# Optimization experiments

Hardware: AMD Instinct MI355X
Metric: run time of the kernel (lower is better)

The kernel has to match this reference:

```python
import jax, jax.numpy as jnp
import numpy as np
import math

S, B, H, NH, I, L, V, BK, MP = 512, 8, 768, 12, 2304, 4, 16384, 32, 512
DH = H // NH   # 64
DV = I // NH   # 192
EPS = 1e-7
SCALE = 1.0 / math.sqrt(3 * DH)


def make_log_bucket_position(relative_pos, bucket_size, max_position):
    sign = np.sign(relative_pos)
    mid = bucket_size // 2
    abs_pos = np.where((relative_pos < mid) & (relative_pos > -mid),
                       mid - 1,
                       np.clip(np.abs(relative_pos), None, max_position - 1))
    log_pos = np.ceil(np.log(abs_pos / mid) / math.log((max_position - 1) / mid) * (mid - 1)).astype(np.int64) + mid
    bucket_pos = np.where(abs_pos <= mid, relative_pos, log_pos * sign).astype(np.int64)
    return bucket_pos


def layer_norm(x, eps=EPS):
    m = jnp.mean(x, axis=-1, keepdims=True)
    v = jnp.var(x, axis=-1, keepdims=True)
    return (x - m) / jnp.sqrt(v + eps)


def setup_inputs() -> dict:
    key = jax.random.key(0)
    ks = jax.random.split(key, 10)
    std = math.sqrt(2.0 / (5.0 * H))
    inp = {}
    inp['input_ids'] = jax.random.randint(ks[0], (S, B), 0, V, dtype=jnp.int32)
    inp['attention_mask'] = jnp.zeros((B, 1, 1, S), dtype=bool)
    rel = np.arange(S)[:, None] - np.arange(S)[None, :]
    rel = make_log_bucket_position(rel, BK, MP)
    inp['position_indices'] = jnp.asarray(BK - 1 + rel, dtype=jnp.int32)  # [S,S] in [0, 2*BK-2]
    inp['word_emb'] = jax.random.normal(ks[1], (V, H), jnp.float32) * std
    inp['rel_emb'] = jax.random.normal(ks[2], (2 * BK - 1, H), jnp.float32) * std
    inp['rel_ln_w'] = jnp.ones((H,), jnp.float32)
    inp['rel_ln_b'] = jnp.zeros((H,), jnp.float32)
    inp['Wv'] = jax.random.normal(ks[3], (L, 2 * I, H), jnp.float32) * std
    inp['Wqk'] = jax.random.normal(ks[4], (L, 2 * H, H), jnp.float32) * std
    inp['bqk'] = jnp.zeros((L, 2 * H), jnp.float32)
    inp['Wo'] = jax.random.normal(ks[5], (L, H, I), jnp.float32) * std
    inp['l_skip'] = jnp.zeros((L, I), jnp.float32)
    return inp


def attention_glu_layer(x, mask, rel, pos_idx, Wv, Wqk, bqk, Wo, l_skip):
    # x: [S,B,H]; rel: [2*BK-1, H]; mask: [B,1,1,S] bool (True = masked)
    h = layer_norm(x)
    vg = jnp.einsum('sbh,ih->sbi', h, Wv)                  # [S,B,2I]
    value, gate = jnp.split(vg, 2, axis=-1)
    gate = jax.nn.gelu(gate, approximate=False)
    value_skip = jax.nn.gelu(value, approximate=False)
    qk = jnp.einsum('sbh,ih->sbi', h, Wqk) + bqk            # [S,B,2H]
    q, k = jnp.split(qk, 2, axis=-1)
    # relative position projections
    pos = rel @ Wqk.T + bqk                                 # [2*BK-1, 2H]
    pos = pos[pos_idx]                                      # [S,S,2H]
    q_pos, k_pos = jnp.split(pos, 2, axis=-1)
    q_pos = q_pos.reshape(S, S, NH, DH)
    k_pos = k_pos.reshape(S, S, NH, DH)
    q4 = q.reshape(S, B, NH, DH)
    k4 = k.reshape(S, B, NH, DH)
    v4 = value.reshape(S, B, NH, DV)
    scores = jnp.einsum('qbhd,kbhd->bhqk', q4, k4) * SCALE
    scores = scores + jnp.einsum('qbhd,qkhd->bhqk', q4, k_pos) * SCALE
    scores = scores + jnp.einsum('kbhd,qkhd->bhqk', k4, q_pos) * SCALE
    scores = jnp.where(mask, -jnp.inf, scores)
    probs = jax.nn.softmax(scores, axis=-1)
    probs = jnp.where(mask, 0.0, probs)
    ctx = jnp.einsum('bhqk,kbhv->qbhv', probs, v4).reshape(S, B, I)
    ctx = ctx + jax.nn.sigmoid(l_skip) * value_skip
    ctx = ctx * gate
    ctx = layer_norm(ctx)
    out = jnp.einsum('sbi,hi->sbh', ctx, Wo)
    return x + out


def reference(input_ids, attention_mask, position_indices, word_emb, rel_emb,
              rel_ln_w, rel_ln_b, Wv, Wqk, bqk, Wo, l_skip):
    x = layer_norm(word_emb[input_ids])                      # [S,B,H]
    rel = layer_norm(rel_emb) * rel_ln_w + rel_ln_b          # [2*BK-1, H]
    for l in range(L):
        x = attention_glu_layer(x, attention_mask, rel, position_indices,
                                Wv[l], Wqk[l], bqk[l], Wo[l], l_skip[l])
    return x
```

## Files before the change

kernel.cpp:

```cpp
#include <hip/hip_runtime.h>
#include <hip/hip_bf16.h>
#include <math.h>

#define S 512
#define B 8
#define H 768
#define NH 12
#define DH 64
#define DV 192
#define II 2304
#define NL 4
#define SCALE 0.07216878364870322f
#define EPS 1e-7f

#define NW0 (2*II*H)
#define NW1 (2*H*H)
#define NW2 (H*II)

typedef __attribute__((ext_vector_type(8))) short short8;
typedef __attribute__((ext_vector_type(4))) float f32x4;

__device__ __forceinline__ float b2f(ushort u){
  union { float f; unsigned int u; } v; v.u = ((unsigned int)u) << 16; return v.f;
}
__device__ __forceinline__ ushort f2b(float f){
  union { float f; unsigned int u; } v; v.f = f;
  unsigned int u = v.u;
  return (ushort)((u + 0x7fffu + ((u >> 16) & 1u)) >> 16);
}
__device__ __forceinline__ float gelu_f(float x){
  return 0.5f * x * (1.0f + erff(x * 0.70710678118654752f));
}
__device__ __forceinline__ void async_copy16(const ushort* g, ushort* l){
  __builtin_amdgcn_global_load_lds(
      (const __attribute__((address_space(1))) void*)g,
      (__attribute__((address_space(3))) void*)l, 16, 0, 0);
}

__device__ __forceinline__ void block_sum2(float& s, float& s2, float* red, int t){
  #pragma unroll
  for(int off=32; off>=1; off>>=1){ s += __shfl_xor(s, off); s2 += __shfl_xor(s2, off); }
  int w = t >> 6;
  if((t & 63) == 0){ red[w] = s; red[4 + w] = s2; }
  __syncthreads();
  s  = red[0] + red[1] + red[2] + red[3];
  s2 = red[4] + red[5] + red[6] + red[7];
}

__global__ __launch_bounds__(256)
void f2b3_kernel(const float* __restrict__ in0, const float* __restrict__ in1,
                 const float* __restrict__ in2, ushort* __restrict__ out){
  int i = (blockIdx.x * 256 + threadIdx.x) * 4;
  const float* src; int off;
  if(i < NW0){ src = in0; off = i; }
  else if(i < NW0+NW1){ src = in1; off = i - NW0; }
  else { src = in2; off = i - NW0 - NW1; }
  float4 v = *(const float4*)(src + off);
  __attribute__((aligned(8))) ushort tmp[4] = { f2b(v.x), f2b(v.y), f2b(v.z), f2b(v.w) };
  *(uint2*)(out + i) = *(const uint2*)tmp;
}

__global__ __launch_bounds__(256)
void embed_ln_kernel(const int* __restrict__ ids, const float* __restrict__ wemb,
                     float* __restrict__ x)
{
  __shared__ float red[8];
  const int sb = blockIdx.x, t = threadIdx.x;
  const float* row = wemb + (size_t)ids[sb] * H;
  float v0 = row[t], v1 = row[t+256], v2 = row[t+512];
  float s = v0+v1+v2, s2 = v0*v0+v1*v1+v2*v2;
  block_sum2(s, s2, red, t);
  float mean = s * (1.0f/H);
  float rstd = rsqrtf(s2*(1.0f/H) - mean*mean + EPS);
  float* xo = x + (size_t)sb * H;
  xo[t]     = (v0-mean)*rstd;
  xo[t+256] = (v1-mean)*rstd;
  xo[t+512] = (v2-mean)*rstd;
}

__global__ __launch_bounds__(256)
void rel_ln_kernel(const float* __restrict__ rel_emb, const float* __restrict__ w,
                   const float* __restrict__ bia, ushort* __restrict__ outb)
{
  __shared__ float red[8];
  const int j = blockIdx.x, t = threadIdx.x;
  const float* row = rel_emb + (size_t)j * H;
  float v0=row[t], v1=row[t+256], v2=row[t+512];
  float s=v0+v1+v2, s2=v0*v0+v1*v1+v2*v2;
  block_sum2(s,s2,red,t);
  float mean = s*(1.0f/H);
  float rstd = rsqrtf(s2*(1.0f/H)-mean*mean+EPS);
  ushort* o = outb + (size_t)j*H;
  o[t]     = f2b((v0-mean)*rstd * w[t]     + bia[t]);
  o[t+256] = f2b((v1-mean)*rstd * w[t+256] + bia[t+256]);
  o[t+512] = f2b((v2-mean)*rstd * w[t+512] + bia[t+512]);
}

__global__ __launch_bounds__(256)
void ln_x_kernel(const float* __restrict__ x, ushort* __restrict__ h)
{
  __shared__ float red[8];
  const int sb = blockIdx.x, t = threadIdx.x;
  const float* row = x + (size_t)sb * H;
  float v0 = row[t], v1 = row[t+256], v2 = row[t+512];
  float s = v0+v1+v2, s2 = v0*v0+v1*v1+v2*v2;
  block_sum2(s, s2, red, t);
  float mean = s * (1.0f/H);
  float rstd = rsqrtf(s2*(1.0f/H) - mean*mean + EPS);
  ushort* o = h + (size_t)sb * H;
  o[t]     = f2b((v0-mean)*rstd);
  o[t+256] = f2b((v1-mean)*rstd);
  o[t+512] = f2b((v2-mean)*rstd);
}

__global__ __launch_bounds__(256)
void bucket_kernel(const int* __restrict__ pidx, unsigned char* __restrict__ buk){
  int r = blockIdx.x*256 + threadIdx.x;
  int rel = r - 511;
  int v = 0;
  if(rel <= 0)          v = pidx[-rel];
  else if(rel <= 511)   v = pidx[511*S + (511-rel)];
  buk[r] = (unsigned char)v;
}

__global__ __launch_bounds__(256)
void gemm_nt64(const ushort* __restrict__ A, const ushort* __restrict__ Bw,
               const float* __restrict__ bias, ushort* __restrict__ Cout,
               int M, int N, int K)
{
  __shared__ ushort As[64][40];
  __shared__ ushort Bs[64][40];
  const int n0 = blockIdx.x * 64, m0 = blockIdx.y * 64;
  const int t = threadIdx.x;
  const int lrow = t >> 2, lk = (t & 3) * 8;
  const int lane = t & 63, w = t >> 6, lr = lane & 15, lq = lane >> 4;
  const int wr = (w >> 1) * 32, wc = (w & 1) * 32;
  f32x4 z = {0.f,0.f,0.f,0.f};
  f32x4 acc[2][2] = {{z,z},{z,z}};
  const int arow = m0 + lrow;
  const ushort* aptr = A  + (size_t)arow * K + lk;
  const ushort* bptr = Bw + (size_t)(n0 + lrow) * K + lk;
  for(int k0 = 0; k0 < K; k0 += 32){
    short8 av = {0,0,0,0,0,0,0,0};
    if(arow < M) av = *(const short8*)(aptr + k0);
    short8 bv = *(const short8*)(bptr + k0);
    __syncthreads();
    *(short8*)&As[lrow][lk] = av;
    *(short8*)&Bs[lrow][lk] = bv;
    __syncthreads();
    short8 a0 = *(const short8*)&As[wr + lr][lq * 8];
    short8 a1 = *(const short8*)&As[wr + 16 + lr][lq * 8];
    short8 b0 = *(const short8*)&Bs[wc + lr][lq * 8];
    short8 b1 = *(const short8*)&Bs[wc + 16 + lr][lq * 8];
    acc[0][0] = __builtin_amdgcn_mfma_f32_16x16x32_bf16(a0, b0, acc[0][0], 0,0,0);
    acc[0][1] = __builtin_amdgcn_mfma_f32_16x16x32_bf16(a0, b1, acc[0][1], 0,0,0);
    acc[1][0] = __builtin_amdgcn_mfma_f32_16x16x32_bf16(a1, b0, acc[1][0], 0,0,0);
    acc[1][1] = __builtin_amdgcn_mfma_f32_16x16x32_bf16(a1, b1, acc[1][1], 0,0,0);
  }
  #pragma unroll
  for(int i=0;i<2;i++){
    #pragma unroll
    for(int j=0;j<2;j++){
      #pragma unroll
      for(int r=0;r<4;r++){
        int m = m0 + wr + i*16 + lq*4 + r;
        int n = n0 + wc + j*16 + lr;
        if(m >= M) continue;
        float v = acc[i][j][r];
        if(bias) v += bias[n];
        Cout[(size_t)m*N + n] = f2b(v);
      }
    }
  }
}

template<int OUT_MODE>
__global__ __launch_bounds__(256)
void gemm128(const ushort* __restrict__ A, const ushort* __restrict__ Bw,
             const float* __restrict__ bias, void* __restrict__ Cout,
             int M, int N, int K)
{
  __shared__ ushort As[2][128*32];
  __shared__ ushort Bs[2][128*32];
  const int t = threadIdx.x, w = t>>6, lane = t&63, lr = lane&15, lq = lane>>4;
  const int m0 = blockIdx.y*128, n0 = blockIdx.x*128;
  const int wr = (w>>1)*64, wc = (w&1)*64;
  const int srow = (w*2)*16 + (lane>>2);
  const int sk = (lane&3)*8;
  const ushort* aG = A  + (size_t)(m0+srow)*K + sk;
  const ushort* bG = Bw + (size_t)(n0+srow)*K + sk;
  f32x4 z = {0.f,0.f,0.f,0.f};
  f32x4 acc[4][4] = {{z,z,z,z},{z,z,z,z},{z,z,z,z},{z,z,z,z}};
  for(int k0 = 0; k0 < K; k0 += 64){
    __syncthreads();
    #pragma unroll
    for(int s=0;s<2;s++){
      async_copy16(aG + k0 + s*32,                 As[s] + (w*2)*512);
      async_copy16(aG + k0 + s*32 + (size_t)16*K,  As[s] + (w*2+1)*512);
      async_copy16(bG + k0 + s*32,                 Bs[s] + (w*2)*512);
      async_copy16(bG + k0 + s*32 + (size_t)16*K,  Bs[s] + (w*2+1)*512);
    }
    __syncthreads();
    #pragma unroll
    for(int s=0;s<2;s++){
      short8 af[4], bf[4];
      #pragma unroll
      for(int i=0;i<4;i++) af[i] = *(const short8*)&As[s][(wr + i*16 + lr)*32 + lq*8];
      #pragma unroll
      for(int j=0;j<4;j++) bf[j] = *(const short8*)&Bs[s][(wc + j*16 + lr)*32 + lq*8];
      #pragma unroll
      for(int i=0;i<4;i++)
        #pragma unroll
        for(int j=0;j<4;j++)
          acc[i][j] = __builtin_amdgcn_mfma_f32_16x16x32_bf16(af[i], bf[j], acc[i][j], 0,0,0);
    }
  }
  #pragma unroll
  for(int i=0;i<4;i++){
    #pragma unroll
    for(int j=0;j<4;j++){
      #pragma unroll
      for(int r=0;r<4;r++){
        int m = m0 + wr + i*16 + lq*4 + r;
        int n = n0 + wc + j*16 + lr;
        float v = acc[i][j][r];
        if(bias) v += bias[n];
        if(OUT_MODE == 0)      ((float*) Cout)[(size_t)m*N + n] = v;
        else if(OUT_MODE == 1) ((ushort*)Cout)[(size_t)m*N + n] = f2b(v);
        else                   ((float*) Cout)[(size_t)m*N + n] += v;
      }
    }
  }
}

#define VGQK_TILE(KT, CUR, SB) do {                                            \
    const int ks0_ = ((KT)+2)*64;                                              \
    const bool do_stage_ = ((KT)+2) < NT;                                      \
    if((KT) < NT-1) asm volatile("s_waitcnt vmcnt(6)" ::: "memory");           \
    else            asm volatile("s_waitcnt vmcnt(0)" ::: "memory");           \
    __builtin_amdgcn_s_barrier();                                              \
    __builtin_amdgcn_sched_barrier(0);                                         \
    short8 bfr_[4][2], afr_[2][2];                                             \
    _Pragma("unroll")                                                          \
    for(int j=0;j<4;j++)                                                       \
      _Pragma("unroll")                                                        \
      for(int ks=0;ks<2;ks++)                                                  \
        bfr_[j][ks] = *(const short8*)&(CUR)[8192 + (wn*64 + j*16 + lr)*64 + ((ks*32 + lq*8) ^ rxor)]; \
    _Pragma("unroll")                                                          \
    for(int i=0;i<2;i++)                                                       \
      _Pragma("unroll")                                                        \
      for(int ks=0;ks<2;ks++)                                                  \
        afr_[i][ks] = *(const short8*)&(CUR)[(wm*64 + i*16 + lr)*64 + ((ks*32 + lq*8) ^ rxor)]; \
    if(do_stage_){                                                             \
      async_copy16(aSrc + ks0_,                (SB) + dA);                     \
      async_copy16(aSrc + (size_t)64*K + ks0_, (SB) + 4096 + dA);              \
      async_copy16(bSrc + ks0_,                (SB) + 8192 + dA);              \
    }                                                                          \
    __builtin_amdgcn_s_barrier();                                              \
    asm volatile("s_waitcnt lgkmcnt(0)" ::: "memory");                         \
    __builtin_amdgcn_sched_barrier(0);                                         \
    __builtin_amdgcn_s_setprio(1);                                             \
    _Pragma("unroll")                                                          \
    for(int i=0;i<2;i++)                                                       \
      _Pragma("unroll")                                                        \
      for(int j=0;j<4;j++)                                                     \
        _Pragma("unroll")                                                      \
        for(int ks=0;ks<2;ks++)                                                \
          acc[i][j] = __builtin_amdgcn_mfma_f32_16x16x32_bf16(afr_[i][ks], bfr_[j][ks], acc[i][j], 0,0,0); \
    __builtin_amdgcn_s_setprio(0);                                             \
    __builtin_amdgcn_s_barrier();                                              \
    __builtin_amdgcn_sched_barrier(0);                                         \
    short8 afr2_[2][2];                                                        \
    _Pragma("unroll")                                                          \
    for(int i=0;i<2;i++)                                                       \
      _Pragma("unroll")                                                        \
      for(int ks=0;ks<2;ks++)                                                  \
        afr2_[i][ks] = *(const short8*)&(CUR)[(wm*64 + (2+i)*16 + lr)*64 + ((ks*32 + lq*8) ^ rxor)]; \
    if(do_stage_){                                                             \
      async_copy16(bSrc + (size_t)64*K + ks0_,  (SB) + 12288 + dA);            \
      async_copy16(bSrc + (size_t)128*K + ks0_, (SB) + 16384 + dA);            \
      async_copy16(bSrc + (size_t)192*K + ks0_, (SB) + 20480 + dA);            \
    }                                                                          \
    __builtin_amdgcn_s_barrier();                                              \
    asm volatile("s_waitcnt lgkmcnt(0)" ::: "memory");                         \
    __builtin_amdgcn_sched_barrier(0);                                         \
    __builtin_amdgcn_s_setprio(1);                                             \
    _Pragma("unroll")                                                          \
    for(int i=0;i<2;i++)                                                       \
      _Pragma("unroll")                                                        \
      for(int j=0;j<4;j++)                                                     \
        _Pragma("unroll")                                                      \
        for(int ks=0;ks<2;ks++)                                                \
          acc[2+i][j] = __builtin_amdgcn_mfma_f32_16x16x32_bf16(afr2_[i][ks], bfr_[j][ks], acc[2+i][j], 0,0,0); \
    __builtin_amdgcn_s_setprio(0);                                             \
  } while(0)

__global__ __launch_bounds__(512)
void gemm_vgqk8(const ushort* __restrict__ A, const ushort* __restrict__ Ww,
                const float* __restrict__ bqk, ushort* __restrict__ vg,
                ushort* __restrict__ qk)
{
  constexpr int K  = H;
  constexpr int NT = K / 64;
  __shared__ ushort buf0[24576];
  __shared__ ushort buf1[24576];
  __shared__ ushort buf2[24576];
  const int t = threadIdx.x;
  const int w = t >> 6, l = t & 63, lr = l & 15, lq = l >> 4;
  const int wm = w >> 2, wn = w & 3;
  int id = blockIdx.x;
  int swz = (id & 7) * 96 + (id >> 3);
  const int bm = swz & 31, bn = swz >> 5;
  const int m0 = bm * 128, n0 = bn * 256;

  const int srow = l >> 3;
  const int scol = ((l & 7) ^ srow) << 3;
  const ushort* aSrc = A  + (size_t)(m0 + w*8 + srow) * K + scol;
  const ushort* bSrc = Ww + (size_t)(n0 + w*8 + srow) * K + scol;
  const int dA = w * 512;
  const int rxor = (lr & 7) << 3;

  f32x4 z = {0.f,0.f,0.f,0.f};
  f32x4 acc[4][4] = {{z,z,z,z},{z,z,z,z},{z,z,z,z},{z,z,z,z}};

  async_copy16(aSrc + 0,                  buf0 + dA);
  async_copy16(aSrc + (size_t)64*K + 0,   buf0 + 4096  + dA);
  async_copy16(bSrc + 0,                  buf0 + 8192  + dA);
  async_copy16(bSrc + (size_t)64*K + 0,   buf0 + 12288 + dA);
  async_copy16(bSrc + (size_t)128*K + 0,  buf0 + 16384 + dA);
  async_copy16(bSrc + (size_t)192*K + 0,  buf0 + 20480 + dA);
  async_copy16(aSrc + 64,                 buf1 + dA);
  async_copy16(aSrc + (size_t)64*K + 64,  buf1 + 4096  + dA);
  async_copy16(bSrc + 64,                 buf1 + 8192  + dA);
  async_copy16(bSrc + (size_t)64*K + 64,  buf1 + 12288 + dA);
  async_copy16(bSrc + (size_t)128*K + 64, buf1 + 16384 + dA);
  async_copy16(bSrc + (size_t)192*K + 64, buf1 + 20480 + dA);

  for(int m3=0; m3<NT/3; m3++){
    const int kt = m3*3;
    VGQK_TILE(kt,   buf0, buf2);
    VGQK_TILE(kt+1, buf1, buf0);
    VGQK_TILE(kt+2, buf2, buf1);
  }

  const bool is_qk = (n0 >= 2*II);
  #pragma unroll
  for(int i=0;i<4;i++){
    #pragma unroll
    for(int j=0;j<4;j++){
      #pragma unroll
      for(int r=0;r<4;r++){
        int m = m0 + wm*64 + i*16 + lq*4 + r;
        int n = n0 + wn*64 + j*16 + lr;
        float v = acc[i][j][r];
        if(is_qk){
          int nq = n - 2*II;
          qk[(size_t)m*(2*H) + nq] = f2b(v + bqk[nq]);
        } else {
          vg[(size_t)m*(2*II) + n] = f2b(v);
        }
      }
    }
  }
}

__global__ __launch_bounds__(256)
void vtcpq_kernel(const ushort* __restrict__ vg, ushort* __restrict__ vt,
                  const ushort* __restrict__ qk, const ushort* __restrict__ posb,
                  ushort* __restrict__ cpT, ushort* __restrict__ cqT,
                  ushort* __restrict__ kT)
{
  const int id = blockIdx.x;
  const int t = threadIdx.x;
  __shared__ ushort tile[32][200];
  if(id < 1536){
    const int st = id & 15;
    const int hh = (id >> 4) % 12;
    const int b  = id / 192;
    {
      int sl = t >> 3, v0 = (t & 7) * 24;
      const ushort* src = vg + ((size_t)((st*32 + sl)*B + b))*(2*II) + hh*DV + v0;
      *(short8*)&tile[sl][v0]      = *(const short8*)(src);
      *(short8*)&tile[sl][v0 + 8]  = *(const short8*)(src + 8);
      *(short8*)&tile[sl][v0 + 16] = *(const short8*)(src + 16);
    }
    __syncthreads();
    if(t < DV){
      __attribute__((aligned(16))) ushort tmp[32];
      #pragma unroll
      for(int s2=0;s2<32;s2++) tmp[s2] = tile[s2][t];
      ushort* dst = vt + ((((size_t)(b*NH + hh))*16 + st)*DV + t)*32;
      #pragma unroll
      for(int c=0;c<32;c+=8) *(short8*)(dst + c) = *(const short8*)&tmp[c];
    }
  } else if(id < 2304){
    const int jid = id - 1536;
    const int kc = jid & 3;
    const int bh = (jid >> 2) % 96;
    const int which = jid / 384;
    const int bb = bh / NH, h = bh - bb*NH;
    const int w = t>>6, lane = t&63, lr = lane&15, lq = lane>>4;
    const ushort* ab = posb + (size_t)(w*16 + lr)*1536 + (which ? 0 : 768) + h*64;
    short8 a0 = *(const short8*)(ab + lq*8);
    short8 a1 = *(const short8*)(ab + 32 + lq*8);
    f32x4 z = {0.f,0.f,0.f,0.f};
    f32x4 acc[8] = {z,z,z,z,z,z,z,z};
    #pragma unroll
    for(int nt=0; nt<8; nt++){
      const int k = kc*128 + nt*16 + lr;
      const ushort* bp = qk + ((size_t)k*B + bb)*1536 + (which ? 768 : 0) + h*64;
      short8 b0 = *(const short8*)(bp + lq*8);
      short8 b1 = *(const short8*)(bp + 32 + lq*8);
      acc[nt] = __builtin_amdgcn_mfma_f32_16x16x32_bf16(a0, b0, acc[nt], 0,0,0);
      acc[nt] = __builtin_amdgcn_mfma_f32_16x16x32_bf16(a1, b1, acc[nt], 0,0,0);
    }
    ushort* outp = which ? cqT : cpT;
    #pragma unroll
    for(int nt=0; nt<8; nt++){
      #pragma unroll
      for(int r=0;r<4;r++){
        int j = w*16 + lq*4 + r;
        int k = kc*128 + nt*16 + lr;
        outp[((size_t)bh*64 + j)*512 + k] = f2b(acc[nt][r]);
      }
    }
  } else {
    const int id2 = id - 2304;
    const int bb = id2 / NH, hh = id2 - bb*NH;
    const int sl = t >> 3, d0 = (t & 7) * 8;
    const ushort* srcb = qk + (size_t)bb*1536 + H + hh*64 + d0;
    ushort* dstb = kT + ((size_t)id2*512 + sl)*64 + d0;
    #pragma unroll
    for(int i=0;i<16;i++){
      int s = i*32 + sl;
      *(short8*)(dstb + (size_t)i*32*64) = *(const short8*)(srcb + (size_t)s*B*1536);
    }
  }
}

__global__ __launch_bounds__(256)
void attn_kernel(const ushort* __restrict__ qk, const ushort* __restrict__ vt,
                 const ushort* __restrict__ kT,
                 const ushort* __restrict__ cpT, const ushort* __restrict__ cqT,
                 const unsigned char* __restrict__ bukg, ushort* __restrict__ ctx)
{
  const int bh = blockIdx.x, qt = blockIdx.y;
  const int b = bh / NH, hh = bh - b*NH;
  __shared__ ushort Qs[32][72];
  __shared__ float  cps[32][65];
  __shared__ ushort cqslab[32*520];
  __shared__ unsigned char bukl[1024];
  __shared__ float redm[4][32];
  __shared__ float reds[4][32];
  __shared__ float rowinv[32];
  const int t = threadIdx.x, w = t>>6, lane = t&63, lr = lane&15, lq = lane>>4;

  ((uint*)bukl)[t] = ((const uint*)bukg)[t & 255];
  for(int i=t; i<512; i+=256){
    int r = i >> 4, d0 = (i & 15) * 4;
    const ushort* src = qk + ((size_t)((qt*32 + r)*B + b))*1536 + hh*DH + d0;
    *(uint2*)&Qs[r][d0] = *(const uint2*)src;
  }
  for(int i=t; i<32*64; i+=256){
    int j = i >> 5, r = i & 31;
    cps[r][j] = b2f(cpT[((size_t)bh*64 + j)*512 + qt*32 + r]);
  }
  __syncthreads();

  const ushort* cqbase = cqT + (size_t)bh*64*512;
  #pragma unroll 8
  for(int n=0; n<64; n++){
    int i = n*256 + t;
    int k = i & 511, q = i >> 9;
    int pi = (int)bukl[(qt*32 + q) - k + 511];
    cqslab[q*520 + k] = cqbase[(size_t)pi*512 + k];
  }
  __syncthreads();

  short8 a00 = *(const short8*)&Qs[lr][lq*8];
  short8 a01 = *(const short8*)&Qs[lr][32 + lq*8];
  short8 a10 = *(const short8*)&Qs[16 + lr][lq*8];
  short8 a11 = *(const short8*)&Qs[16 + lr][32 + lq*8];

  float sc[8][8];
  const int kbase = w * 128;
  const ushort* ktb = kT + (size_t)bh*512*64;
  f32x4 z4 = {0.f,0.f,0.f,0.f};
  #pragma unroll
  for(int tile=0; tile<8; tile++){
    const int k0 = kbase + tile*16;
    const ushort* kp = ktb + (size_t)(k0 + lr)*64 + lq*8;
    short8 b0 = *(const short8*)kp;
    short8 b1 = *(const short8*)(kp + 32);
    f32x4 acc[2] = {z4, z4};
    acc[0] = __builtin_amdgcn_mfma_f32_16x16x32_bf16(a00, b0, acc[0], 0,0,0);
    acc[0] = __builtin_amdgcn_mfma_f32_16x16x32_bf16(a01, b1, acc[0], 0,0,0);
    acc[1] = __builtin_amdgcn_mfma_f32_16x16x32_bf16(a10, b0, acc[1], 0,0,0);
    acc[1] = __builtin_amdgcn_mfma_f32_16x16x32_bf16(a11, b1, acc[1], 0,0,0);
    const int kcol = k0 + lr;
    #pragma unroll
    for(int qs=0;qs<2;qs++){
      #pragma unroll
      for(int r=0;r<4;r++){
        int ql = qs*16 + lq*4 + r;
        int pi = (int)bukl[(qt*32 + ql) - kcol + 511];
        sc[tile][qs*4+r] = (acc[qs][r] + cps[ql][pi]
                       + b2f(cqslab[ql*520 + kcol])) * SCALE;
      }
    }
  }

  float gm[8];
  #pragma unroll
  for(int j=0;j<8;j++){
    float m = sc[0][j];
    #pragma unroll
    for(int tile=1;tile<8;tile++) m = fmaxf(m, sc[tile][j]);
    #pragma unroll
    for(int off=1; off<16; off<<=1) m = fmaxf(m, __shfl_xor(m, off));
    if(lr==0) redm[w][(j>>2)*16 + lq*4 + (j&3)] = m;
  }
  __syncthreads();
  #pragma unroll
  for(int j=0;j<8;j++){
    int ql = (j>>2)*16 + lq*4 + (j&3);
    gm[j] = fmaxf(fmaxf(redm[0][ql],redm[1][ql]),fmaxf(redm[2][ql],redm[3][ql]));
  }
  #pragma unroll
  for(int j=0;j<8;j++){
    float s = 0.f;
    #pragma unroll
    for(int tile=0;tile<8;tile++){ float e = __expf(sc[tile][j]-gm[j]); sc[tile][j]=e; s+=e; }
    #pragma unroll
    for(int off=1; off<16; off<<=1) s += __shfl_xor(s, off);
    if(lr==0) reds[w][(j>>2)*16 + lq*4 + (j&3)] = s;
  }
  __syncthreads();
  #pragma unroll
  for(int j=0;j<8;j++){
    int ql = (j>>2)*16 + lq*4 + (j&3);
    float g = reds[0][ql]+reds[1][ql]+reds[2][ql]+reds[3][ql];
    if(w==0 && lr==0) rowinv[ql] = 1.0f/g;
  }
  ushort* Psp = cqslab;
  #pragma unroll
  for(int tile=0;tile<8;tile++){
    #pragma unroll
    for(int j=0;j<8;j++){
      int ql = (j>>2)*16 + lq*4 + (j&3);
      Psp[ql*520 + kbase + tile*16 + lr] = f2b(sc[tile][j]);
    }
  }
  __syncthreads();

  f32x4 acc2[2][3] = {{z4,z4,z4},{z4,z4,z4}};
  const ushort* vbh = vt + (size_t)bh*16*DV*32;
  #pragma unroll 4
  for(int kk=0; kk<S; kk+=32){
    short8 p0 = *(const short8*)&Psp[lr*520 + kk + lq*8];
    short8 p1 = *(const short8*)&Psp[(16 + lr)*520 + kk + lq*8];
    const ushort* vslab = vbh + (size_t)(kk>>5)*DV*32;
    #pragma unroll
    for(int ti=0; ti<3; ti++){
      const int v0 = (w*3 + ti)*16;
      short8 bv = *(const short8*)(vslab + (size_t)(v0 + lr)*32 + lq*8);
      acc2[0][ti] = __builtin_amdgcn_mfma_f32_16x16x32_bf16(p0, bv, acc2[0][ti], 0,0,0);
      acc2[1][ti] = __builtin_amdgcn_mfma_f32_16x16x32_bf16(p1, bv, acc2[1][ti], 0,0,0);
    }
  }
  #pragma unroll
  for(int qs=0;qs<2;qs++){
    #pragma unroll
    for(int ti=0; ti<3; ti++){
      const int v0 = (w*3 + ti)*16;
      #pragma unroll
      for(int r=0;r<4;r++){
        int ql = qs*16 + lq*4 + r;
        float val = acc2[qs][ti][r] * rowinv[ql];
        ctx[((size_t)((qt*32+ql)*B + b))*II + hh*DV + v0 + lr] = f2b(val);
      }
    }
  }
}

__global__ __launch_bounds__(256)
void glu_ln_kernel(const ushort* __restrict__ ctx, const ushort* __restrict__ vg,
                   const float* __restrict__ ls, ushort* __restrict__ outb)
{
  __shared__ float red[8];
  const int sb = blockIdx.x, t = threadIdx.x;
  const ushort* crow = ctx + (size_t)sb*II;
  const ushort* vrow = vg + (size_t)sb*2*II;
  float c[9]; float s=0.f, s2=0.f;
  #pragma unroll
  for(int i=0;i<9;i++){
    int idx = t + i*256;
    float cv  = b2f(crow[idx]);
    float val = b2f(vrow[idx]);
    float gt  = b2f(vrow[II + idx]);
    float sk  = 1.0f/(1.0f + __expf(-ls[idx]));
    cv = (cv + sk*gelu_f(val)) * gelu_f(gt);
    c[i]=cv; s+=cv; s2+=cv*cv;
  }
  block_sum2(s,s2,red,t);
  float mean = s*(1.0f/II);
  float rstd = rsqrtf(s2*(1.0f/II)-mean*mean+EPS);
  ushort* o = outb + (size_t)sb*II;
  #pragma unroll
  for(int i=0;i<9;i++) o[t+i*256] = f2b((c[i]-mean)*rstd);
}

__global__ __launch_bounds__(256)
void copy_kernel(const float* __restrict__ x, float* __restrict__ out){
  int i = (blockIdx.x*256 + threadIdx.x)*4;
  *(float4*)(out + i) = *(const float4*)(x + i);
}

extern "C" void kernel_launch(void* const* d_in, const int* in_sizes, int n_in,
                              void* d_out, int out_size, void* d_ws, size_t ws_size,
                              hipStream_t stream)
{
  (void)in_sizes; (void)n_in; (void)out_size; (void)ws_size;
  const int* ids      = (const int*)d_in[0];
  const int* pidx     = (const int*)d_in[2];
  const float* wemb   = (const float*)d_in[3];
  const float* rele   = (const float*)d_in[4];
  const float* rlw    = (const float*)d_in[5];
  const float* rlb    = (const float*)d_in[6];
  const float* Wv     = (const float*)d_in[7];
  const float* Wqk    = (const float*)d_in[8];
  const float* bqk    = (const float*)d_in[9];
  const float* Wo     = (const float*)d_in[10];
  const float* lskip  = (const float*)d_in[11];

  char* wsb = (char*)d_ws;
  float*  x     = (float*) (wsb + 0);
  ushort* h     = (ushort*)(wsb + 12582912);
  ushort* relb  = (ushort*)(wsb + 18874368);
  ushort* posb  = (ushort*)(wsb + 18972672);
  ushort* vg    = (ushort*)(wsb + 19169280);
  ushort* qk    = (ushort*)(wsb + 56918016);
  ushort* cpT   = (ushort*)(wsb + 69500928);
  ushort* cqT   = (ushort*)(wsb + 75792384);
  ushort* ctx   = (ushort*)(wsb + 82083840);
  ushort* vt    = (ushort*)(wsb + 100958208);
  ushort* ctxln = vt;
  ushort* wvqk  = (ushort*)(wsb + 119832576);
  ushort* wqkb  = wvqk + (size_t)NW0;
  ushort* wob   = wvqk + (size_t)(NW0 + NW1);
  ushort* kT    = h;
  unsigned char* bukg = (unsigned char*)(posb + 63*1536);

  embed_ln_kernel<<<S*B, 256, 0, stream>>>(ids, wemb, x);
  rel_ln_kernel<<<63, 256, 0, stream>>>(rele, rlw, rlb, relb);
  bucket_kernel<<<4, 256, 0, stream>>>(pidx, bukg);

  for(int l=0; l<NL; l++){
    const float* Wv_l  = Wv  + (size_t)l * NW0;
    const float* Wqk_l = Wqk + (size_t)l * NW1;
    const float* bqk_l = bqk + (size_t)l * (2*H);
    const float* Wo_l  = Wo  + (size_t)l * NW2;
    const float* ls_l  = lskip + (size_t)l * II;

    f2b3_kernel<<<(NW0+NW1+NW2)/1024, 256, 0, stream>>>(Wv_l, Wqk_l, Wo_l, wvqk);
    ln_x_kernel<<<S*B, 256, 0, stream>>>(x, h);
    gemm_nt64<<<dim3((2*H)/64, 1), 256, 0, stream>>>(relb, wqkb, bqk_l, posb, 63, 2*H, H);
    gemm_vgqk8<<<768, 512, 0, stream>>>(h, wvqk, bqk_l, vg, qk);
    vtcpq_kernel<<<2400, 256, 0, stream>>>(vg, vt, qk, posb, cpT, cqT, kT);
    attn_kernel<<<dim3(B*NH, S/32), 256, 0, stream>>>(qk, vt, kT, cpT, cqT, bukg, ctx);
    glu_ln_kernel<<<S*B, 256, 0, stream>>>(ctx, vg, ls_l, ctxln);
    gemm128<2><<<dim3(H/128, (S*B)/128), 256, 0, stream>>>(ctxln, wob, nullptr, x, S*B, H, II);
  }
  copy_kernel<<<(S*B*H)/1024, 256, 0, stream>>>(x, (float*)d_out);
}
```

Baseline: 1.237 ms.

## Replace 128x256 triple-buffered VG/QK GEMM with 128x128 double-buffered tiles

The fused value/gate/QK projection GEMM now uses 128x128 output tiles with 256-thread blocks and two LDS buffers, in place of 128x256 tiles with 512 threads and a three-stage pipeline. It also drops the split-phase scheduling: the interleaved barriers, the explicit waitcnt control and the setprio hints. The smaller tiles double the grid and cut LDS use per block, which should raise occupancy and help load balance across CUs. In exchange, B-operand reuse per block is lower and global-to-LDS latency hiding is shallower.

New measurement: 1.236 ms. Within noise of the previous version (-0.1%).

```diff
diff --git a/kernel.cpp b/kernel.cpp
--- a/kernel.cpp
+++ b/kernel.cpp
@@ -233,114 +233,76 @@
   }
 }
 
-#define VGQK_TILE(KT, CUR, SB) do {                                            \
-    const int ks0_ = ((KT)+2)*64;                                              \
-    const bool do_stage_ = ((KT)+2) < NT;                                      \
-    if((KT) < NT-1) asm volatile("s_waitcnt vmcnt(6)" ::: "memory");           \
-    else            asm volatile("s_waitcnt vmcnt(0)" ::: "memory");           \
-    __builtin_amdgcn_s_barrier();                                              \
-    __builtin_amdgcn_sched_barrier(0);                                         \
-    short8 bfr_[4][2], afr_[2][2];                                             \
+#define VGQK9_STAGE(KT, SA, SB) do {                                           \
+    const int k0_ = (KT)*64;                                                   \
+    async_copy16(aSrc + k0_,                 (SA) + dA);                       \
+    async_copy16(aSrc + (size_t)32*K + k0_,  (SA) + 2048  + dA);               \
+    async_copy16(aSrc + (size_t)64*K + k0_,  (SA) + 4096  + dA);               \
+    async_copy16(aSrc + (size_t)96*K + k0_,  (SA) + 6144  + dA);               \
+    async_copy16(bSrc + k0_,                 (SB) + dA);                       \
+    async_copy16(bSrc + (size_t)32*K + k0_,  (SB) + 2048  + dA);               \
+    async_copy16(bSrc + (size_t)64*K + k0_,  (SB) + 4096  + dA);               \
+    async_copy16(bSrc + (size_t)96*K + k0_,  (SB) + 6144  + dA);               \
+  } while(0)
+
+#define VGQK9_TILE(KT, CA, CB, SA, SB) do {                                    \
+    __syncthreads();                                                           \
+    if((KT)+1 < NT) VGQK9_STAGE((KT)+1, SA, SB);                               \
+    short8 af_[4][2], bf_[4][2];                                               \
+    _Pragma("unroll")                                                          \
+    for(int i=0;i<4;i++)                                                       \
+      _Pragma("unroll")                                                        \
+      for(int ks=0;ks<2;ks++)                                                  \
+        af_[i][ks] = *(const short8*)&(CA)[(wr + i*16 + lr)*64 + ((ks*32 + lq*8) ^ rxor)]; \
     _Pragma("unroll")                                                          \
     for(int j=0;j<4;j++)                                                       \
       _Pragma("unroll")                                                        \
       for(int ks=0;ks<2;ks++)                                                  \
-        bfr_[j][ks] = *(const short8*)&(CUR)[8192 + (wn*64 + j*16 + lr)*64 + ((ks*32 + lq*8) ^ rxor)]; \
+        bf_[j][ks] = *(const short8*)&(CB)[(wc + j*16 + lr)*64 + ((ks*32 + lq*8) ^ rxor)]; \
     _Pragma("unroll")                                                          \
-    for(int i=0;i<2;i++)                                                       \
-      _Pragma("unroll")                                                        \
-      for(int ks=0;ks<2;ks++)                                                  \
-        afr_[i][ks] = *(const short8*)&(CUR)[(wm*64 + i*16 + lr)*64 + ((ks*32 + lq*8) ^ rxor)]; \
-    if(do_stage_){                                                             \
-      async_copy16(aSrc + ks0_,                (SB) + dA);                     \
-      async_copy16(aSrc + (size_t)64*K + ks0_, (SB) + 4096 + dA);              \
-      async_copy16(bSrc + ks0_,                (SB) + 8192 + dA);              \
-    }                                                                          \
-    __builtin_amdgcn_s_barrier();                                              \
-    asm volatile("s_waitcnt lgkmcnt(0)" ::: "memory");                         \
-    __builtin_amdgcn_sched_barrier(0);                                         \
-    __builtin_amdgcn_s_setprio(1);                                             \
-    _Pragma("unroll")                                                          \
-    for(int i=0;i<2;i++)                                                       \
+    for(int i=0;i<4;i++)                                                       \
       _Pragma("unroll")                                                        \
       for(int j=0;j<4;j++)                                                     \
         _Pragma("unroll")                                                      \
         for(int ks=0;ks<2;ks++)                                                \
-          acc[i][j] = __builtin_amdgcn_mfma_f32_16x16x32_bf16(afr_[i][ks], bfr_[j][ks], acc[i][j], 0,0,0); \
-    __builtin_amdgcn_s_setprio(0);                                             \
-    __builtin_amdgcn_s_barrier();                                              \
-    __builtin_amdgcn_sched_barrier(0);                                         \
-    short8 afr2_[2][2];                                                        \
-    _Pragma("unroll")                                                          \
-    for(int i=0;i<2;i++)                                                       \
-      _Pragma("unroll")                                                        \
-      for(int ks=0;ks<2;ks++)                                                  \
-        afr2_[i][ks] = *(const short8*)&(CUR)[(wm*64 + (2+i)*16 + lr)*64 + ((ks*32 + lq*8) ^ rxor)]; \
-    if(do_stage_){                                                             \
-      async_copy16(bSrc + (size_t)64*K + ks0_,  (SB) + 12288 + dA);            \
-      async_copy16(bSrc + (size_t)128*K + ks0_, (SB) + 16384 + dA);            \
-      async_copy16(bSrc + (size_t)192*K + ks0_, (SB) + 20480 + dA);            \
-    }                                                                          \
-    __builtin_amdgcn_s_barrier();                                              \
-    asm volatile("s_waitcnt lgkmcnt(0)" ::: "memory");                         \
-    __builtin_amdgcn_sched_barrier(0);                                         \
-    __builtin_amdgcn_s_setprio(1);                                             \
-    _Pragma("unroll")                                                          \
-    for(int i=0;i<2;i++)                                                       \
-      _Pragma("unroll")                                                        \
-      for(int j=0;j<4;j++)                                                     \
-        _Pragma("unroll")                                                      \
-        for(int ks=0;ks<2;ks++)                                                \
-          acc[2+i][j] = __builtin_amdgcn_mfma_f32_16x16x32_bf16(afr2_[i][ks], bfr_[j][ks], acc[2+i][j], 0,0,0); \
-    __builtin_amdgcn_s_setprio(0);                                             \
+          acc[i][j] = __builtin_amdgcn_mfma_f32_16x16x32_bf16(af_[i][ks], bf_[j][ks], acc[i][j], 0,0,0); \
   } while(0)
 
-__global__ __launch_bounds__(512)
-void gemm_vgqk8(const ushort* __restrict__ A, const ushort* __restrict__ Ww,
+__global__ __launch_bounds__(256)
+void gemm_vgqk9(const ushort* __restrict__ A, const ushort* __restrict__ Ww,
                 const float* __restrict__ bqk, ushort* __restrict__ vg,
                 ushort* __restrict__ qk)
 {
   constexpr int K  = H;
   constexpr int NT = K / 64;
-  __shared__ ushort buf0[24576];
-  __shared__ ushort buf1[24576];
-  __shared__ ushort buf2[24576];
+  __shared__ ushort As0[8192];
+  __shared__ ushort Bs0[8192];
+  __shared__ ushort As1[8192];
+  __shared__ ushort Bs1[8192];
   const int t = threadIdx.x;
   const int w = t >> 6, l = t & 63, lr = l & 15, lq = l >> 4;
-  const int wm = w >> 2, wn = w & 3;
+  const int wr = (w >> 1) * 64, wc = (w & 1) * 64;
   int id = blockIdx.x;
-  int swz = (id & 7) * 96 + (id >> 3);
+  int swz = (id & 7) * 192 + (id >> 3);
   const int bm = swz & 31, bn = swz >> 5;
-  const int m0 = bm * 128, n0 = bn * 256;
-
-  const int srow = l >> 3;
-  const int scol = ((l & 7) ^ srow) << 3;
-  const ushort* aSrc = A  + (size_t)(m0 + w*8 + srow) * K + scol;
-  const ushort* bSrc = Ww + (size_t)(n0 + w*8 + srow) * K + scol;
+  const int m0 = bm * 128, n0 = bn * 128;
+
+  const int srow = t >> 3;
+  const int scol = ((t & 7) ^ (srow & 7)) << 3;
+  const ushort* aSrc = A  + (size_t)(m0 + srow) * K + scol;
+  const ushort* bSrc = Ww + (size_t)(n0 + srow) * K + scol;
   const int dA = w * 512;
   const int rxor = (lr & 7) << 3;
 
   f32x4 z = {0.f,0.f,0.f,0.f};
   f32x4 acc[4][4] = {{z,z,z,z},{z,z,z,z},{z,z,z,z},{z,z,z,z}};
 
-  async_copy16(aSrc + 0,                  buf0 + dA);
-  async_copy16(aSrc + (size_t)64*K + 0,   buf0 + 4096  + dA);
-  async_copy16(bSrc + 0,                  buf0 + 8192  + dA);
-  async_copy16(bSrc + (size_t)64*K + 0,   buf0 + 12288 + dA);
-  async_copy16(bSrc + (size_t)128*K + 0,  buf0 + 16384 + dA);
-  async_copy16(bSrc + (size_t)192*K + 0,  buf0 + 20480 + dA);
-  async_copy16(aSrc + 64,                 buf1 + dA);
-  async_copy16(aSrc + (size_t)64*K + 64,  buf1 + 4096  + dA);
-  async_copy16(bSrc + 64,                 buf1 + 8192  + dA);
-  async_copy16(bSrc + (size_t)64*K + 64,  buf1 + 12288 + dA);
-  async_copy16(bSrc + (size_t)128*K + 64, buf1 + 16384 + dA);
-  async_copy16(bSrc + (size_t)192*K + 64, buf1 + 20480 + dA);
-
-  for(int m3=0; m3<NT/3; m3++){
-    const int kt = m3*3;
-    VGQK_TILE(kt,   buf0, buf2);
-    VGQK_TILE(kt+1, buf1, buf0);
-    VGQK_TILE(kt+2, buf2, buf1);
+  VGQK9_STAGE(0, As0, Bs0);
+
+  for(int m2 = 0; m2 < NT/2; m2++){
+    const int kt = 2*m2;
+    VGQK9_TILE(kt,   As0, Bs0, As1, Bs1);
+    VGQK9_TILE(kt+1, As1, Bs1, As0, Bs0);
   }
 
   const bool is_qk = (n0 >= 2*II);
@@ -350,8 +312,8 @@
     for(int j=0;j<4;j++){
       #pragma unroll
       for(int r=0;r<4;r++){
-        int m = m0 + wm*64 + i*16 + lq*4 + r;
-        int n = n0 + wn*64 + j*16 + lr;
+        int m = m0 + wr + i*16 + lq*4 + r;
+        int n = n0 + wc + j*16 + lr;
         float v = acc[i][j][r];
         if(is_qk){
           int nq = n - 2*II;
@@ -665,7 +627,7 @@
     f2b3_kernel<<<(NW0+NW1+NW2)/1024, 256, 0, stream>>>(Wv_l, Wqk_l, Wo_l, wvqk);
     ln_x_kernel<<<S*B, 256, 0, stream>>>(x, h);
     gemm_nt64<<<dim3((2*H)/64, 1), 256, 0, stream>>>(relb, wqkb, bqk_l, posb, 63, 2*H, H);
-    gemm_vgqk8<<<768, 512, 0, stream>>>(h, wvqk, bqk_l, vg, qk);
+    gemm_vgqk9<<<1536, 256, 0, stream>>>(h, wvqk, bqk_l, vg, qk);
     vtcpq_kernel<<<2400, 256, 0, stream>>>(vg, vt, qk, posb, cpT, cqT, kT);
     attn_kernel<<<dim3(B*NH, S/32), 256, 0, stream>>>(qk, vt, kT, cpT, cqT, bukg, ctx);
     glu_ln_kernel<<<S*B, 256, 0, stream>>>(ctx, vg, ls_l, ctxln);
```
